# Optimization experiments

Measured on AMD Instinct MI355X. Metric: run time of the kernel, lower is better.

The kernel has to match this reference:

```python
import jax, jax.numpy as jnp
import numpy as np

S, B, D, N, DH = 2048, 2, 1024, 16, 64  # seq, batch, d_model, n_head, d_head
LN_EPS = 1e-5


def setup_inputs() -> dict:
    key = jax.random.key(0)
    ks = jax.random.split(key, 8)
    h = jax.random.normal(ks[0], (S, B, D), dtype=jnp.float32)
    Wq = jax.random.normal(ks[1], (D, N * DH), dtype=jnp.float32) * 0.02
    Wkv = jax.random.normal(ks[2], (D, 2 * N * DH), dtype=jnp.float32) * 0.02
    Wo = jax.random.normal(ks[3], (N * DH, D), dtype=jnp.float32) * 0.02
    ln_gamma = jnp.ones((D,), dtype=jnp.float32)
    ln_beta = jnp.zeros((D,), dtype=jnp.float32)
    # persistent compressive-memory state from a previous segment
    memory = jax.random.normal(ks[4], (B, N, DH, DH), dtype=jnp.float32)
    # normalization is a sum of (elu(k)+1) over ~S positions -> strictly positive, O(S)
    mem_norm = jax.random.uniform(ks[5], (B, 1, N, DH), dtype=jnp.float32) * S + 1.0
    gate_beta = jnp.ones((1,), dtype=jnp.float32) * 0.01  # beta_eps
    return {"h": h, "Wq": Wq, "Wkv": Wkv, "Wo": Wo, "ln_gamma": ln_gamma,
            "ln_beta": ln_beta, "memory": memory, "mem_norm": mem_norm,
            "gate_beta": gate_beta}


def reference(h, Wq, Wkv, Wo, ln_gamma, ln_beta, memory, mem_norm, gate_beta):
    scale = 1.0 / np.sqrt(DH).astype(np.float32)
    # projections (pre_lnorm=False, mems=None -> c == h)
    q = (h @ Wq).reshape(S, B, N, DH)
    k, v = jnp.split(h @ Wkv, 2, axis=-1)
    k = k.reshape(S, B, N, DH)
    v = v.reshape(S, B, N, DH)
    # local quadratic attention
    score = jnp.einsum('ibnd,jbnd->ijbn', q, k) * scale  # [S,S,B,N]
    prob = jax.nn.softmax(score, axis=1)
    attn_vec = jnp.einsum('ijbn,jbnd->ibnd', prob, v).reshape(S, B, N * DH)
    # memory retrieval (NOTE: source swaps K/V in the _update_memory call;
    # it is done under no_grad -> stop_gradient here)
    cached_Q = jax.nn.elu(q.swapaxes(0, 1)) + 1.0          # [B,S,N,DH]
    num = jnp.einsum('bsnk,bnkv->bsnv', cached_Q, memory)   # [B,S,N,DH]
    den = jnp.einsum('bsnk,bvnk->bsnv', cached_Q, mem_norm)  # [B,S,N,1]
    content_A = jax.lax.stop_gradient(num / den)            # [B,S,N,DH]
    # gated injection
    g = jax.nn.sigmoid(gate_beta)                           # [1]
    inj = g * content_A.swapaxes(0, 1).reshape(S, B, N * DH) + (1.0 - g) * attn_vec
    attn_out = inj @ Wo
    # post layernorm residual
    y = h + attn_out
    mu = jnp.mean(y, axis=-1, keepdims=True)
    var = jnp.mean((y - mu) ** 2, axis=-1, keepdims=True)
    return (y - mu) / jnp.sqrt(var + LN_EPS) * ln_gamma + ln_beta
```

## Files before the change

### kernel.cpp

```cpp
#include <hip/hip_runtime.h>


typedef unsigned short ushort_t;
typedef unsigned int uint32;

typedef __bf16 bf16x8 __attribute__((ext_vector_type(8)));
typedef float f32x4 __attribute__((ext_vector_type(4)));
typedef float f32x16 __attribute__((ext_vector_type(16)));
typedef unsigned short u16x8 __attribute__((ext_vector_type(8)));
typedef unsigned short u16x4 __attribute__((ext_vector_type(4)));
typedef unsigned int u32x4 __attribute__((ext_vector_type(4)));

typedef const __attribute__((address_space(1))) void gvoid_t;
typedef __attribute__((address_space(3))) void lvoid_t;

#define S_LEN 2048
#define BATCH 2
#define NHEAD 16

__device__ __forceinline__ ushort_t f2bf(float x) {
  union { float f; unsigned u; } c; c.f = x;
  unsigned r = (c.u + 0x7FFFu + ((c.u >> 16) & 1u)) >> 16;
  return (ushort_t)r;
}
__device__ __forceinline__ float bf2f(ushort_t v) {
  union { unsigned u; float f; } c; c.u = ((unsigned)v) << 16;
  return c.f;
}

__global__ __launch_bounds__(256) void k_cvt_h(const float* __restrict__ src,
                                               ushort_t* __restrict__ dst, int n4) {
  int idx = blockIdx.x * 256 + threadIdx.x;
  if (idx >= n4) return;
  float4 v = ((const float4*)src)[idx];
  u16x4 o; o[0] = f2bf(v.x); o[1] = f2bf(v.y); o[2] = f2bf(v.z); o[3] = f2bf(v.w);
  ((u16x4*)dst)[idx] = o;
}

__global__ __launch_bounds__(256) void k_cvt_wT(const float* __restrict__ W,
                                                ushort_t* __restrict__ WT, int K, int N) {
  __shared__ float tile[32][33];
  const int n0 = blockIdx.x * 32, k0 = blockIdx.y * 32;
  const int tx = threadIdx.x & 31, ty = threadIdx.x >> 5;
#pragma unroll
  for (int r = 0; r < 32; r += 8)
    tile[ty + r][tx] = W[(size_t)(k0 + ty + r) * N + n0 + tx];
  __syncthreads();
#pragma unroll
  for (int r = 0; r < 32; r += 8)
    WT[(size_t)(n0 + ty + r) * K + k0 + tx] = f2bf(tile[tx][ty + r]);
}

template <int OUT_BF16>
__global__ __launch_bounds__(256) void k_gemm_bt(const ushort_t* __restrict__ A,
                                                 const ushort_t* __restrict__ B,
                                                 void* __restrict__ Cv, int M, int N, int K,
                                                 int nbx) {
  __shared__ __attribute__((aligned(16))) ushort_t As[128 * 32];
  __shared__ __attribute__((aligned(16))) ushort_t Bs[128 * 32];
  const int per = gridDim.x >> 3;
  const int fl = (blockIdx.x & 7) * per + (blockIdx.x >> 3);
  const int m0 = (fl / nbx) * 128, n0 = (fl % nbx) * 128;
  const int tid = threadIdx.x, w = tid >> 6, lane = tid & 63;
  const int wm = (w >> 1) * 64, wn = (w & 1) * 64;
  const int l15 = lane & 15, l4 = lane >> 4;
  f32x4 acc[4][4];
#pragma unroll
  for (int i = 0; i < 4; ++i)
#pragma unroll
    for (int j = 0; j < 4; ++j)
#pragma unroll
      for (int r = 0; r < 4; ++r) acc[i][j][r] = 0.f;

  for (int k0 = 0; k0 < K; k0 += 32) {
    __syncthreads();
#pragma unroll
    for (int r = 0; r < 2; ++r) {
      int c = r * 256 + w * 64 + lane;
      const ushort_t* ga = A + (size_t)(m0 + (c >> 2)) * K + k0 + (c & 3) * 8;
      const ushort_t* gb = B + (size_t)(n0 + (c >> 2)) * K + k0 + (c & 3) * 8;
      __builtin_amdgcn_global_load_lds((gvoid_t*)ga, (lvoid_t*)(As + (r * 256 + w * 64) * 8), 16, 0, 0);
      __builtin_amdgcn_global_load_lds((gvoid_t*)gb, (lvoid_t*)(Bs + (r * 256 + w * 64) * 8), 16, 0, 0);
    }
    __syncthreads();
    bf16x8 af[4], bfr[4];
#pragma unroll
    for (int i = 0; i < 4; ++i) af[i] = *(const bf16x8*)&As[(wm + i * 16 + l15) * 32 + l4 * 8];
#pragma unroll
    for (int j = 0; j < 4; ++j) bfr[j] = *(const bf16x8*)&Bs[(wn + j * 16 + l15) * 32 + l4 * 8];
#pragma unroll
    for (int i = 0; i < 4; ++i)
#pragma unroll
      for (int j = 0; j < 4; ++j)
        acc[i][j] = __builtin_amdgcn_mfma_f32_16x16x32_bf16(af[i], bfr[j], acc[i][j], 0, 0, 0);
  }
#pragma unroll
  for (int i = 0; i < 4; ++i)
#pragma unroll
    for (int j = 0; j < 4; ++j)
#pragma unroll
      for (int r = 0; r < 4; ++r) {
        int row = m0 + wm + i * 16 + l4 * 4 + r;
        int col = n0 + wn + j * 16 + l15;
        if (OUT_BF16)
          ((ushort_t*)Cv)[(size_t)row * N + col] = f2bf(acc[i][j][r]);
        else
          ((float*)Cv)[(size_t)row * N + col] = acc[i][j][r];
      }
}

__global__ __launch_bounds__(256) void k_gemm64(const ushort_t* __restrict__ A,
                                                const ushort_t* __restrict__ B,
                                                float* __restrict__ C, int M, int N, int K,
                                                int nbx) {
  __shared__ __attribute__((aligned(16))) ushort_t As[64 * 32];
  __shared__ __attribute__((aligned(16))) ushort_t Bs[128 * 32];
  const int per = gridDim.x >> 3;
  const int fl = (blockIdx.x & 7) * per + (blockIdx.x >> 3);
  const int m0 = (fl / nbx) * 64, n0 = (fl % nbx) * 128;
  const int tid = threadIdx.x, w = tid >> 6, lane = tid & 63;
  const int wn = w * 32;
  const int l15 = lane & 15, l4 = lane >> 4;
  f32x4 acc[4][2];
#pragma unroll
  for (int i = 0; i < 4; ++i)
#pragma unroll
    for (int j = 0; j < 2; ++j)
#pragma unroll
      for (int r = 0; r < 4; ++r) acc[i][j][r] = 0.f;

  for (int k0 = 0; k0 < K; k0 += 32) {
    __syncthreads();
    {
      int c = w * 64 + lane;
      const ushort_t* ga = A + (size_t)(m0 + (c >> 2)) * K + k0 + (c & 3) * 8;
      __builtin_amdgcn_global_load_lds((gvoid_t*)ga, (lvoid_t*)(As + w * 512), 16, 0, 0);
#pragma unroll
      for (int r = 0; r < 2; ++r) {
        int c2 = r * 256 + w * 64 + lane;
        const ushort_t* gb = B + (size_t)(n0 + (c2 >> 2)) * K + k0 + (c2 & 3) * 8;
        __builtin_amdgcn_global_load_lds((gvoid_t*)gb, (lvoid_t*)(Bs + r * 2048 + w * 512), 16, 0, 0);
      }
    }
    __syncthreads();
    bf16x8 af[4], bfr[2];
#pragma unroll
    for (int i = 0; i < 4; ++i) af[i] = *(const bf16x8*)&As[(i * 16 + l15) * 32 + l4 * 8];
#pragma unroll
    for (int j = 0; j < 2; ++j) bfr[j] = *(const bf16x8*)&Bs[(wn + j * 16 + l15) * 32 + l4 * 8];
#pragma unroll
    for (int i = 0; i < 4; ++i)
#pragma unroll
      for (int j = 0; j < 2; ++j)
        acc[i][j] = __builtin_amdgcn_mfma_f32_16x16x32_bf16(af[i], bfr[j], acc[i][j], 0, 0, 0);
  }
#pragma unroll
  for (int i = 0; i < 4; ++i)
#pragma unroll
    for (int j = 0; j < 2; ++j)
#pragma unroll
      for (int r = 0; r < 4; ++r)
        C[(size_t)(m0 + i * 16 + l4 * 4 + r) * N + n0 + wn + j * 16 + l15] = acc[i][j][r];
}

__device__ __forceinline__ void stage_k(const ushort_t* __restrict__ qkv, ushort_t* kw,
                                        int j0, int b, int n, int w, int lane) {
#pragma unroll
  for (int r = 0; r < 2; ++r) {
    int jb_ = w * 16 + r * 8;
    const ushort_t* ksrc = qkv + (size_t)(j0 + jb_ + (lane >> 3)) * 6144 + b * 3072 + n * 64 + 1024
                           + (((lane & 7) ^ (lane >> 3)) << 3);
    __builtin_amdgcn_global_load_lds((gvoid_t*)ksrc, (lvoid_t*)(kw + jb_ * 64), 16, 0, 0);
  }
}

__global__ __launch_bounds__(256) void k_attn(const ushort_t* __restrict__ qkv,
                                              const float* __restrict__ mem,
                                              const float* __restrict__ mnorm,
                                              const float* __restrict__ gbeta,
                                              ushort_t* __restrict__ inj) {
  __shared__ __attribute__((aligned(16))) ushort_t Ks[2][4096];
  __shared__ __attribute__((aligned(16))) ushort_t VTs[2][4096];
  const int bn = blockIdx.y, b = bn & 1, n = bn >> 1;
  const int tid = threadIdx.x, w = tid >> 6, lane = tid & 63;
  const int l31 = lane & 31, h = lane >> 5;
  const int qrow = blockIdx.x * 128 + w * 32 + l31;
  const size_t qoff = (size_t)qrow * 6144 + b * 3072 + n * 64;
  const float CEXP = 0.18033688011113723f;
  bf16x8 qf[4];
#pragma unroll
  for (int ks = 0; ks < 4; ++ks) {
    u16x8 qv = *(const u16x8*)(qkv + qoff + ks * 16 + h * 8);
    union { u16x8 u; bf16x8 v; } cu;
#pragma unroll
    for (int e = 0; e < 8; ++e) cu.u[e] = f2bf(bf2f(qv[e]) * CEXP);
    qf[ks] = cu.v;
  }

  const int vj = tid >> 2, vdq = (tid & 3) * 16, a2 = (tid & 3) * 2;
  const size_t vbase = (size_t)b * 3072 + n * 64 + 2048 + vdq;
  const int krd = l31 & 7;
  const int fv0 = (l31 & 7) ^ (l31 >> 3);
  const int fv1 = fv0 ^ 4;

  stage_k(qkv, Ks[0], 0, b, n, w, lane);
  {
    u16x8 vr0 = *(const u16x8*)(qkv + (size_t)vj * 6144 + vbase);
    u16x8 vr1 = *(const u16x8*)(qkv + (size_t)vj * 6144 + vbase + 8);
#pragma unroll
    for (int e = 0; e < 8; ++e) {
      int f0 = (e ^ a2) << 3;
      VTs[0][(vdq + e) * 64 + (vj ^ f0)] = vr0[e];
      VTs[0][(vdq + 8 + e) * 64 + (vj ^ f0 ^ 8)] = vr1[e];
    }
  }
  __syncthreads();

  f32x16 oacc[2];
#pragma unroll
  for (int r = 0; r < 16; ++r) { oacc[0][r] = 0.f; oacc[1][r] = 0.f; }
  float l_run = 0.f;

  for (int t = 0; t < 32; ++t) {
    const ushort_t* Kb = Ks[t & 1];
    const ushort_t* Vb = VTs[t & 1];
    u16x8 nv0, nv1;
    if (t < 31) {
      stage_k(qkv, Ks[(t + 1) & 1], (t + 1) * 64, b, n, w, lane);
      const ushort_t* vsrc = qkv + (size_t)((t + 1) * 64 + vj) * 6144 + vbase;
      nv0 = *(const u16x8*)vsrc;
      nv1 = *(const u16x8*)(vsrc + 8);
    }
    f32x16 sv[2];
#pragma unroll
    for (int r = 0; r < 16; ++r) { sv[0][r] = 0.f; sv[1][r] = 0.f; }
    __builtin_amdgcn_s_setprio(1);
#pragma unroll
    for (int jb = 0; jb < 2; ++jb) {
      const int rb = (jb * 32 + l31) * 64;
#pragma unroll
      for (int ks = 0; ks < 4; ++ks) {
        bf16x8 kf = *(const bf16x8*)&Kb[rb + ((((ks << 1) | h) ^ krd) << 3)];
        sv[jb] = __builtin_amdgcn_mfma_f32_32x32x16_bf16(kf, qf[ks], sv[jb], 0, 0, 0);
      }
    }
    __builtin_amdgcn_s_setprio(0);
    float p[32];
#pragma unroll
    for (int jb = 0; jb < 2; ++jb)
#pragma unroll
      for (int r = 0; r < 16; ++r)
        p[jb * 16 + r] = __builtin_amdgcn_exp2f(sv[jb][r]);
#pragma unroll
    for (int ks = 0; ks < 4; ++ks) {
      const int jb = ks >> 1, q0 = (ks & 1) * 2;
      uint32 X0, X1, Y0, Y1;
      asm volatile("v_cvt_pk_bf16_f32 %0, %1, %2" : "=v"(X0) : "v"(p[jb * 16 + q0 * 4 + 0]), "v"(p[jb * 16 + q0 * 4 + 1]));
      asm volatile("v_cvt_pk_bf16_f32 %0, %1, %2" : "=v"(X1) : "v"(p[jb * 16 + q0 * 4 + 2]), "v"(p[jb * 16 + q0 * 4 + 3]));
      asm volatile("v_cvt_pk_bf16_f32 %0, %1, %2" : "=v"(Y0) : "v"(p[jb * 16 + (q0 + 1) * 4 + 0]), "v"(p[jb * 16 + (q0 + 1) * 4 + 1]));
      asm volatile("v_cvt_pk_bf16_f32 %0, %1, %2" : "=v"(Y1) : "v"(p[jb * 16 + (q0 + 1) * 4 + 2]), "v"(p[jb * 16 + (q0 + 1) * 4 + 3]));
      asm volatile("v_permlane32_swap_b32 %0, %1" : "+v"(X0), "+v"(Y0));
      asm volatile("v_permlane32_swap_b32 %0, %1" : "+v"(X1), "+v"(Y1));
      union { u32x4 u; bf16x8 v; } pf;
      pf.u[0] = X0; pf.u[1] = X1; pf.u[2] = Y0; pf.u[3] = Y1;
      bf16x8 vf0 = *(const bf16x8*)&Vb[l31 * 64 + ((((ks << 1) | h) ^ fv0) << 3)];
      bf16x8 vf1 = *(const bf16x8*)&Vb[(32 + l31) * 64 + ((((ks << 1) | h) ^ fv1) << 3)];
      __builtin_amdgcn_s_setprio(1);
      oacc[0] = __builtin_amdgcn_mfma_f32_32x32x16_bf16(vf0, pf.v, oacc[0], 0, 0, 0);
      oacc[1] = __builtin_amdgcn_mfma_f32_32x32x16_bf16(vf1, pf.v, oacc[1], 0, 0, 0);
      __builtin_amdgcn_s_setprio(0);
    }
    float ls[16];
#pragma unroll
    for (int r = 0; r < 16; ++r) ls[r] = p[r] + p[16 + r];
#pragma unroll
    for (int st = 8; st >= 1; st >>= 1)
#pragma unroll
      for (int r = 0; r < st; ++r) ls[r] += ls[r + st];
    l_run += ls[0] + __shfl_xor(ls[0], 32);
    if (t < 31) {
      ushort_t* Vw = VTs[(t + 1) & 1];
#pragma unroll
      for (int e = 0; e < 8; ++e) {
        int f0 = (e ^ a2) << 3;
        Vw[(vdq + e) * 64 + (vj ^ f0)] = nv0[e];
        Vw[(vdq + 8 + e) * 64 + (vj ^ f0 ^ 8)] = nv1[e];
      }
      __syncthreads();
    }
  }

  float den = 0.f;
  bf16x8 cqf[4];
  const float* nrm = mnorm + (size_t)(b * NHEAD + n) * 64;
#pragma unroll
  for (int ks = 0; ks < 4; ++ks) {
    u16x8 qv = *(const u16x8*)(qkv + qoff + ks * 16 + h * 8);
    union { u16x8 u; bf16x8 v; } cu;
#pragma unroll
    for (int e = 0; e < 8; ++e) {
      float x = bf2f(qv[e]);
      float c = (x > 0.f) ? (x + 1.f) : __builtin_amdgcn_exp2f(x * 1.4426950408889634f);
      cu.u[e] = f2bf(c);
      den += c * nrm[ks * 16 + h * 8 + e];
    }
    cqf[ks] = cu.v;
  }
  den += __shfl_xor(den, 32);

  const float* mb = mem + (size_t)(b * NHEAD + n) * 4096;
  f32x16 accv[2];
#pragma unroll
  for (int r = 0; r < 16; ++r) { accv[0][r] = 0.f; accv[1][r] = 0.f; }
#pragma unroll
  for (int db = 0; db < 2; ++db)
#pragma unroll
    for (int ks = 0; ks < 4; ++ks) {
      union { u16x8 u; bf16x8 v; } af;
#pragma unroll
      for (int e = 0; e < 8; ++e)
        af.u[e] = f2bf(mb[(size_t)(ks * 16 + h * 8 + e) * 64 + db * 32 + l31]);
      accv[db] = __builtin_amdgcn_mfma_f32_32x32x16_bf16(af.v, cqf[ks], accv[db], 0, 0, 0);
    }

  float g = 1.f / (1.f + expf(-gbeta[0]));
  float rden = 1.f / den, invl = 1.f / l_run;
  ushort_t* op = inj + (size_t)qrow * 2048 + b * 1024 + n * 64;
#pragma unroll
  for (int db = 0; db < 2; ++db)
#pragma unroll
    for (int qq = 0; qq < 4; ++qq) {
      u16x4 st;
#pragma unroll
      for (int m = 0; m < 4; ++m) {
        float content = accv[db][qq * 4 + m] * rden;
        float av = oacc[db][qq * 4 + m] * invl;
        st[m] = f2bf(g * content + (1.f - g) * av);
      }
      *(u16x4*)(op + db * 32 + qq * 8 + h * 4) = st;
    }
}

__global__ __launch_bounds__(256) void k_ln(const float* __restrict__ h,
                                            const float* __restrict__ ao,
                                            const float* __restrict__ gam,
                                            const float* __restrict__ bet,
                                            float* __restrict__ out) {
  const int m = blockIdx.x, t = threadIdx.x;
  const int lane = t & 63, w = t >> 6;
  __shared__ float redS[4], redQ[4];
  const size_t base = (size_t)m * 1024;
  float4 hv = ((const float4*)(h + base))[t];
  float4 avv = ((const float4*)(ao + base))[t];
  float y0 = hv.x + avv.x, y1 = hv.y + avv.y, y2 = hv.z + avv.z, y3 = hv.w + avv.w;
  float s = y0 + y1 + y2 + y3;
  float sq = y0 * y0 + y1 * y1 + y2 * y2 + y3 * y3;
#pragma unroll
  for (int mk = 32; mk >= 1; mk >>= 1) { s += __shfl_xor(s, mk); sq += __shfl_xor(sq, mk); }
  if (lane == 0) { redS[w] = s; redQ[w] = sq; }
  __syncthreads();
  float Ssum = redS[0] + redS[1] + redS[2] + redS[3];
  float Qsum = redQ[0] + redQ[1] + redQ[2] + redQ[3];
  float mu = Ssum * (1.f / 1024.f);
  float var = Qsum * (1.f / 1024.f) - mu * mu;
  float rstd = rsqrtf(var + 1e-5f);
  float4 g = ((const float4*)gam)[t];
  float4 bt = ((const float4*)bet)[t];
  float4 o;
  o.x = (y0 - mu) * rstd * g.x + bt.x;
  o.y = (y1 - mu) * rstd * g.y + bt.y;
  o.z = (y2 - mu) * rstd * g.z + bt.z;
  o.w = (y3 - mu) * rstd * g.w + bt.w;
  ((float4*)(out + base))[t] = o;
}

extern "C" void kernel_launch(void* const* d_in, const int* in_sizes, int n_in,
                              void* d_out, int out_size, void* d_ws, size_t ws_size,
                              hipStream_t stream) {
  const float* h = (const float*)d_in[0];
  const float* Wq = (const float*)d_in[1];
  const float* Wkv = (const float*)d_in[2];
  const float* Wo = (const float*)d_in[3];
  const float* gam = (const float*)d_in[4];
  const float* bet = (const float*)d_in[5];
  const float* mem = (const float*)d_in[6];
  const float* mnorm = (const float*)d_in[7];
  const float* gbeta = (const float*)d_in[8];
  float* out = (float*)d_out;

  char* ws = (char*)d_ws;
  ushort_t* hb  = (ushort_t*)(ws);
  ushort_t* wT  = (ushort_t*)(ws + (size_t)(8u << 20));
  ushort_t* woT = (ushort_t*)(ws + (size_t)(14u << 20));
  ushort_t* qkv = (ushort_t*)(ws + (size_t)(16u << 20));
  float*    ao  = (float*)   (ws + (size_t)(16u << 20));
  ushort_t* inj = hb;

  k_cvt_h<<<4096, 256, 0, stream>>>(h, hb, 1048576);
  k_cvt_wT<<<dim3(32, 32), 256, 0, stream>>>(Wq, wT, 1024, 1024);
  k_cvt_wT<<<dim3(64, 32), 256, 0, stream>>>(Wkv, wT + (size_t)1024 * 1024, 1024, 2048);
  k_cvt_wT<<<dim3(32, 32), 256, 0, stream>>>(Wo, woT, 1024, 1024);
  k_gemm_bt<1><<<768, 256, 0, stream>>>(hb, wT, (void*)qkv, 4096, 3072, 1024, 24);
  k_attn<<<dim3(16, 32), 256, 0, stream>>>(qkv, mem, mnorm, gbeta, inj);
  k_gemm64<<<512, 256, 0, stream>>>(inj, woT, ao, 4096, 1024, 1024, 8);
  k_ln<<<4096, 256, 0, stream>>>(h, ao, gam, bet, out);
}
```

Before: 147.4 us.

## Pre-transpose V into a separate buffer and stage it with async LDS loads

Adds a k_vt kernel that writes V transposed per (batch, head) into a workspace buffer. The attention kernel then stages V^T tiles with global_load_lds direct-to-LDS copies, like K, instead of loading V into registers and scattering transposed elements into LDS every iteration. This removes per-iteration VGPR pressure and scalar LDS stores from the inner loop. It costs an extra kernel launch plus a write and re-read of V through global memory. It also reuses the score registers for the exponentials instead of a separate p array.

```diff
diff --git a/kernel.cpp b/kernel.cpp
--- a/kernel.cpp
+++ b/kernel.cpp
@@ -163,6 +163,32 @@
         C[(size_t)(m0 + i * 16 + l4 * 4 + r) * N + n0 + wn + j * 16 + l15] = acc[i][j][r];
 }
 
+__global__ __launch_bounds__(256) void k_vt(const ushort_t* __restrict__ qkv,
+                                            ushort_t* __restrict__ vt) {
+  __shared__ uint32 tile[64 * 65];
+  const int jt = blockIdx.x, bn = blockIdx.y, b = bn & 1, n = bn >> 1;
+  const int tid = threadIdx.x;
+  const int j0 = jt * 64;
+#pragma unroll
+  for (int rr = 0; rr < 2; ++rr) {
+    int lin = rr * 2048 + tid * 8;
+    int j = lin >> 6, d0 = lin & 63;
+    u16x8 v = *(const u16x8*)(qkv + (size_t)(j0 + j) * 6144 + b * 3072 + 2048 + n * 64 + d0);
+#pragma unroll
+    for (int e = 0; e < 8; ++e) tile[j * 65 + d0 + e] = v[e];
+  }
+  __syncthreads();
+#pragma unroll
+  for (int rr = 0; rr < 2; ++rr) {
+    int lin = rr * 2048 + tid * 8;
+    int d = lin >> 6, jj = lin & 63;
+    u16x8 o;
+#pragma unroll
+    for (int e = 0; e < 8; ++e) o[e] = (ushort_t)tile[(jj + e) * 65 + d];
+    *(u16x8*)(vt + ((size_t)bn * 64 + d) * 2048 + j0 + jj) = o;
+  }
+}
+
 __device__ __forceinline__ void stage_k(const ushort_t* __restrict__ qkv, ushort_t* kw,
                                         int j0, int b, int n, int w, int lane) {
 #pragma unroll
@@ -173,8 +199,19 @@
     __builtin_amdgcn_global_load_lds((gvoid_t*)ksrc, (lvoid_t*)(kw + jb_ * 64), 16, 0, 0);
   }
 }
+__device__ __forceinline__ void stage_vt(const ushort_t* __restrict__ vt, ushort_t* vw,
+                                         int j0, int bn, int w, int lane) {
+#pragma unroll
+  for (int r = 0; r < 2; ++r) {
+    int db_ = w * 16 + r * 8;
+    const ushort_t* vsrc = vt + ((size_t)bn * 64 + db_ + (lane >> 3)) * 2048 + j0
+                           + (((lane & 7) ^ (lane >> 3)) << 3);
+    __builtin_amdgcn_global_load_lds((gvoid_t*)vsrc, (lvoid_t*)(vw + db_ * 64), 16, 0, 0);
+  }
+}
 
 __global__ __launch_bounds__(256) void k_attn(const ushort_t* __restrict__ qkv,
+                                              const ushort_t* __restrict__ vt,
                                               const float* __restrict__ mem,
                                               const float* __restrict__ mnorm,
                                               const float* __restrict__ gbeta,
@@ -196,24 +233,10 @@
     for (int e = 0; e < 8; ++e) cu.u[e] = f2bf(bf2f(qv[e]) * CEXP);
     qf[ks] = cu.v;
   }
-
-  const int vj = tid >> 2, vdq = (tid & 3) * 16, a2 = (tid & 3) * 2;
-  const size_t vbase = (size_t)b * 3072 + n * 64 + 2048 + vdq;
   const int krd = l31 & 7;
-  const int fv0 = (l31 & 7) ^ (l31 >> 3);
-  const int fv1 = fv0 ^ 4;
 
   stage_k(qkv, Ks[0], 0, b, n, w, lane);
-  {
-    u16x8 vr0 = *(const u16x8*)(qkv + (size_t)vj * 6144 + vbase);
-    u16x8 vr1 = *(const u16x8*)(qkv + (size_t)vj * 6144 + vbase + 8);
-#pragma unroll
-    for (int e = 0; e < 8; ++e) {
-      int f0 = (e ^ a2) << 3;
-      VTs[0][(vdq + e) * 64 + (vj ^ f0)] = vr0[e];
-      VTs[0][(vdq + 8 + e) * 64 + (vj ^ f0 ^ 8)] = vr1[e];
-    }
-  }
+  stage_vt(vt, VTs[0], 0, bn, w, lane);
   __syncthreads();
 
   f32x16 oacc[2];
@@ -224,12 +247,9 @@
   for (int t = 0; t < 32; ++t) {
     const ushort_t* Kb = Ks[t & 1];
     const ushort_t* Vb = VTs[t & 1];
-    u16x8 nv0, nv1;
     if (t < 31) {
       stage_k(qkv, Ks[(t + 1) & 1], (t + 1) * 64, b, n, w, lane);
-      const ushort_t* vsrc = qkv + (size_t)((t + 1) * 64 + vj) * 6144 + vbase;
-      nv0 = *(const u16x8*)vsrc;
-      nv1 = *(const u16x8*)(vsrc + 8);
+      stage_vt(vt, VTs[(t + 1) & 1], (t + 1) * 64, bn, w, lane);
     }
     f32x16 sv[2];
 #pragma unroll
@@ -245,26 +265,26 @@
       }
     }
     __builtin_amdgcn_s_setprio(0);
-    float p[32];
 #pragma unroll
     for (int jb = 0; jb < 2; ++jb)
 #pragma unroll
       for (int r = 0; r < 16; ++r)
-        p[jb * 16 + r] = __builtin_amdgcn_exp2f(sv[jb][r]);
+        sv[jb][r] = __builtin_amdgcn_exp2f(sv[jb][r]);
 #pragma unroll
     for (int ks = 0; ks < 4; ++ks) {
       const int jb = ks >> 1, q0 = (ks & 1) * 2;
       uint32 X0, X1, Y0, Y1;
-      asm volatile("v_cvt_pk_bf16_f32 %0, %1, %2" : "=v"(X0) : "v"(p[jb * 16 + q0 * 4 + 0]), "v"(p[jb * 16 + q0 * 4 + 1]));
-      asm volatile("v_cvt_pk_bf16_f32 %0, %1, %2" : "=v"(X1) : "v"(p[jb * 16 + q0 * 4 + 2]), "v"(p[jb * 16 + q0 * 4 + 3]));
-      asm volatile("v_cvt_pk_bf16_f32 %0, %1, %2" : "=v"(Y0) : "v"(p[jb * 16 + (q0 + 1) * 4 + 0]), "v"(p[jb * 16 + (q0 + 1) * 4 + 1]));
-      asm volatile("v_cvt_pk_bf16_f32 %0, %1, %2" : "=v"(Y1) : "v"(p[jb * 16 + (q0 + 1) * 4 + 2]), "v"(p[jb * 16 + (q0 + 1) * 4 + 3]));
+      asm volatile("v_cvt_pk_bf16_f32 %0, %1, %2" : "=v"(X0) : "v"(sv[jb][q0 * 4 + 0]), "v"(sv[jb][q0 * 4 + 1]));
+      asm volatile("v_cvt_pk_bf16_f32 %0, %1, %2" : "=v"(X1) : "v"(sv[jb][q0 * 4 + 2]), "v"(sv[jb][q0 * 4 + 3]));
+      asm volatile("v_cvt_pk_bf16_f32 %0, %1, %2" : "=v"(Y0) : "v"(sv[jb][(q0 + 1) * 4 + 0]), "v"(sv[jb][(q0 + 1) * 4 + 1]));
+      asm volatile("v_cvt_pk_bf16_f32 %0, %1, %2" : "=v"(Y1) : "v"(sv[jb][(q0 + 1) * 4 + 2]), "v"(sv[jb][(q0 + 1) * 4 + 3]));
       asm volatile("v_permlane32_swap_b32 %0, %1" : "+v"(X0), "+v"(Y0));
       asm volatile("v_permlane32_swap_b32 %0, %1" : "+v"(X1), "+v"(Y1));
       union { u32x4 u; bf16x8 v; } pf;
       pf.u[0] = X0; pf.u[1] = X1; pf.u[2] = Y0; pf.u[3] = Y1;
-      bf16x8 vf0 = *(const bf16x8*)&Vb[l31 * 64 + ((((ks << 1) | h) ^ fv0) << 3)];
-      bf16x8 vf1 = *(const bf16x8*)&Vb[(32 + l31) * 64 + ((((ks << 1) | h) ^ fv1) << 3)];
+      const int g = ((((ks << 1) | h) ^ krd) << 3);
+      bf16x8 vf0 = *(const bf16x8*)&Vb[l31 * 64 + g];
+      bf16x8 vf1 = *(const bf16x8*)&Vb[(32 + l31) * 64 + g];
       __builtin_amdgcn_s_setprio(1);
       oacc[0] = __builtin_amdgcn_mfma_f32_32x32x16_bf16(vf0, pf.v, oacc[0], 0, 0, 0);
       oacc[1] = __builtin_amdgcn_mfma_f32_32x32x16_bf16(vf1, pf.v, oacc[1], 0, 0, 0);
@@ -272,22 +292,13 @@
     }
     float ls[16];
 #pragma unroll
-    for (int r = 0; r < 16; ++r) ls[r] = p[r] + p[16 + r];
+    for (int r = 0; r < 16; ++r) ls[r] = sv[0][r] + sv[1][r];
 #pragma unroll
     for (int st = 8; st >= 1; st >>= 1)
 #pragma unroll
       for (int r = 0; r < st; ++r) ls[r] += ls[r + st];
     l_run += ls[0] + __shfl_xor(ls[0], 32);
-    if (t < 31) {
-      ushort_t* Vw = VTs[(t + 1) & 1];
-#pragma unroll
-      for (int e = 0; e < 8; ++e) {
-        int f0 = (e ^ a2) << 3;
-        Vw[(vdq + e) * 64 + (vj ^ f0)] = nv0[e];
-        Vw[(vdq + 8 + e) * 64 + (vj ^ f0 ^ 8)] = nv1[e];
-      }
-      __syncthreads();
-    }
+    if (t < 31) __syncthreads();
   }
 
   float den = 0.f;
@@ -394,6 +405,7 @@
   ushort_t* woT = (ushort_t*)(ws + (size_t)(14u << 20));
   ushort_t* qkv = (ushort_t*)(ws + (size_t)(16u << 20));
   float*    ao  = (float*)   (ws + (size_t)(16u << 20));
+  ushort_t* vtb = (ushort_t*)(ws + (size_t)(40u << 20));
   ushort_t* inj = hb;
 
   k_cvt_h<<<4096, 256, 0, stream>>>(h, hb, 1048576);
@@ -401,7 +413,8 @@
   k_cvt_wT<<<dim3(64, 32), 256, 0, stream>>>(Wkv, wT + (size_t)1024 * 1024, 1024, 2048);
   k_cvt_wT<<<dim3(32, 32), 256, 0, stream>>>(Wo, woT, 1024, 1024);
   k_gemm_bt<1><<<768, 256, 0, stream>>>(hb, wT, (void*)qkv, 4096, 3072, 1024, 24);
-  k_attn<<<dim3(16, 32), 256, 0, stream>>>(qkv, mem, mnorm, gbeta, inj);
+  k_vt<<<dim3(32, 32), 256, 0, stream>>>(qkv, vtb);
+  k_attn<<<dim3(16, 32), 256, 0, stream>>>(qkv, vtb, mem, mnorm, gbeta, inj);
   k_gemm64<<<512, 256, 0, stream>>>(inj, woT, ao, 4096, 1024, 1024, 8);
   k_ln<<<4096, 256, 0, stream>>>(h, ao, gam, bet, out);
 }
```

New measurement: 147.0 us. Within noise of the previous version (-0.3%).
